# Kernel tuning notes

Measured on AMD Instinct MI355X. Metric: run time of the kernel, lower is better.

The kernel has to match this reference:

```python
import jax, jax.numpy as jnp
import numpy as np

NUM_PROPERTIES = 10000
HDIM = 512
OUTPUT_DIM = 2
BATCH = 512
NUM_PROPS = 128


def setup_inputs() -> dict:
    key = jax.random.key(0)
    k1, k2, k3, k4 = jax.random.split(key, 4)
    hidden_states = jax.random.normal(k1, (BATCH, NUM_PROPS, HDIM), dtype=jnp.float32)
    properties = jax.random.randint(k2, (BATCH, NUM_PROPS), 0, NUM_PROPERTIES, dtype=jnp.int64)
    mask = jnp.ones((BATCH, NUM_PROPS), dtype=jnp.float32)
    # learned params: per-property classifier weight (H, D) and bias (D)
    classifier_weights = jax.random.normal(k3, (NUM_PROPERTIES, HDIM, OUTPUT_DIM), dtype=jnp.float32) * 0.02
    classifier_bias = jax.random.normal(k4, (NUM_PROPERTIES, OUTPUT_DIM), dtype=jnp.float32) * 0.02
    return {
        "hidden_states": hidden_states,
        "properties": properties,
        "mask": mask,
        "classifier_weights": classifier_weights,
        "classifier_bias": classifier_bias,
    }


def reference(hidden_states, properties, mask, classifier_weights, classifier_bias):
    # gather per-(batch, prop) weight matrices and biases
    W = classifier_weights[properties]          # (B, P, H, D)
    b = classifier_bias[properties]             # (B, P, D)
    # (B,P,1,H) @ (B,P,H,D) -> (B,P,D)
    out = jnp.einsum("bph,bphd->bpd", hidden_states, W) + b
    out = out * mask[..., None]
    return out
```

## Files before the change

### kernel.cpp

```cpp
#include <hip/hip_runtime.h>


#define H 512
#define D 2
#define CAP 48
#define OVF_WAVES 256

__device__ __forceinline__ void gemv_one_bp(
    const float* __restrict__ hs, const float* __restrict__ mask,
    const float* __restrict__ W,  const float* __restrict__ bias,
    float* __restrict__ out, int bp, int prop, int lane)
{
    const float2* h2 = (const float2*)(hs + (size_t)bp * H);
    const float4* w4 = (const float4*)(W + (size_t)prop * (H * D));

    float2 ha = h2[lane];
    float2 hb = h2[64 + lane];
    float2 hc = h2[128 + lane];
    float2 hd = h2[192 + lane];
    float4 wa = w4[lane];
    float4 wb = w4[64 + lane];
    float4 wc = w4[128 + lane];
    float4 wd = w4[192 + lane];

    float s0 = ha.x * wa.x + ha.y * wa.z
             + hb.x * wb.x + hb.y * wb.z
             + hc.x * wc.x + hc.y * wc.z
             + hd.x * wd.x + hd.y * wd.z;
    float s1 = ha.x * wa.y + ha.y * wa.w
             + hb.x * wb.y + hb.y * wb.w
             + hc.x * wc.y + hc.y * wc.w
             + hd.x * wd.y + hd.y * wd.w;

    #pragma unroll
    for (int off = 32; off > 0; off >>= 1) {
        s0 += __shfl_xor(s0, off, 64);
        s1 += __shfl_xor(s1, off, 64);
    }

    if (lane == 0) {
        const float m  = mask[bp];
        const float b0 = bias[(size_t)prop * D + 0];
        const float b1 = bias[(size_t)prop * D + 1];
        float2 r;
        r.x = (s0 + b0) * m;
        r.y = (s1 + b1) * m;
        *(float2*)(out + (size_t)bp * D) = r;
    }
}

__global__ __launch_bounds__(256) void bucket_kernel(
    const int* __restrict__ props, int BP,
    int* __restrict__ counts,
    int* __restrict__ slots,
    int* __restrict__ ovf_cnt,
    int* __restrict__ ovf)
{
    int i = blockIdx.x * blockDim.x + threadIdx.x;
    const int stride = gridDim.x * blockDim.x;
    for (; i < BP; i += stride) {
        const int p = props[i];
        const int idx = atomicAdd(&counts[p], 1);
        if (idx < CAP) {
            slots[p * CAP + idx] = i;
        } else {
            const int o = atomicAdd(ovf_cnt, 1);
            ovf[o] = i;
        }
    }
}

__global__ __launch_bounds__(256) void per_prop_kernel(
    const float* __restrict__ hs,
    const int*   __restrict__ props,
    const float* __restrict__ mask,
    const float* __restrict__ W,
    const float* __restrict__ bias,
    float*       __restrict__ out,
    const int*   __restrict__ counts,
    const int*   __restrict__ slots,
    const int*   __restrict__ ovf_cnt,
    const int*   __restrict__ ovf,
    int nprop)
{
    const int wid  = (blockIdx.x * blockDim.x + threadIdx.x) >> 6;
    const int lane = threadIdx.x & 63;

    if (wid < nprop) {
        int cnt = counts[wid];
        if (cnt > CAP) cnt = CAP;
        if (cnt == 0) return;

        const float4* w4 = (const float4*)(W + (size_t)wid * (H * D));
        const float4 wa = w4[lane];
        const float4 wb = w4[64 + lane];
        const float4 wc = w4[128 + lane];
        const float4 wd = w4[192 + lane];
        const float b0 = bias[(size_t)wid * D + 0];
        const float b1 = bias[(size_t)wid * D + 1];

        const int myslot = (lane < cnt) ? slots[wid * CAP + lane] : 0;

        int bp = __shfl(myslot, 0, 64);
        const float2* h2 = (const float2*)(hs + (size_t)bp * H);
        float2 ha = h2[lane];
        float2 hb = h2[64 + lane];
        float2 hc = h2[128 + lane];
        float2 hd = h2[192 + lane];

        for (int j = 0; j < cnt; ++j) {
            const int bpn = __shfl(myslot, (j + 1 < 64) ? j + 1 : 0, 64);
            float2 na = make_float2(0.f, 0.f), nb = na, nc = na, nd = na;
            if (j + 1 < cnt) {
                const float2* hn = (const float2*)(hs + (size_t)bpn * H);
                na = hn[lane];
                nb = hn[64 + lane];
                nc = hn[128 + lane];
                nd = hn[192 + lane];
            }

            float s0 = ha.x * wa.x + ha.y * wa.z
                     + hb.x * wb.x + hb.y * wb.z
                     + hc.x * wc.x + hc.y * wc.z
                     + hd.x * wd.x + hd.y * wd.z;
            float s1 = ha.x * wa.y + ha.y * wa.w
                     + hb.x * wb.y + hb.y * wb.w
                     + hc.x * wc.y + hc.y * wc.w
                     + hd.x * wd.y + hd.y * wd.w;

            #pragma unroll
            for (int off = 32; off > 0; off >>= 1) {
                s0 += __shfl_xor(s0, off, 64);
                s1 += __shfl_xor(s1, off, 64);
            }

            if (lane == 0) {
                const float m = mask[bp];
                float2 r;
                r.x = (s0 + b0) * m;
                r.y = (s1 + b1) * m;
                *(float2*)(out + (size_t)bp * D) = r;
            }

            bp = bpn;
            ha = na; hb = nb; hc = nc; hd = nd;
        }
    } else {
        const int n = *ovf_cnt;
        for (int i = wid - nprop; i < n; i += OVF_WAVES) {
            const int bp = ovf[i];
            gemv_one_bp(hs, mask, W, bias, out, bp, props[bp], lane);
        }
    }
}

__global__ __launch_bounds__(256) void adapter_gemv_kernel(
    const float* __restrict__ hs,
    const int*   __restrict__ props,
    const float* __restrict__ mask,
    const float* __restrict__ W,
    const float* __restrict__ bias,
    float* __restrict__ out,
    int BP)
{
    const int tid  = blockIdx.x * blockDim.x + threadIdx.x;
    const int bp   = tid >> 6;
    const int lane = tid & 63;
    if (bp >= BP) return;
    gemv_one_bp(hs, mask, W, bias, out, bp, props[bp], lane);
}

extern "C" void kernel_launch(void* const* d_in, const int* in_sizes, int n_in,
                              void* d_out, int out_size, void* d_ws, size_t ws_size,
                              hipStream_t stream) {
    const float* hs    = (const float*)d_in[0];
    const int*   props = (const int*)d_in[1];
    const float* mask  = (const float*)d_in[2];
    const float* W     = (const float*)d_in[3];
    const float* bias  = (const float*)d_in[4];
    float* out = (float*)d_out;

    const int BP    = in_sizes[1];
    const int nprop = in_sizes[3] / (H * D);

    const size_t off_counts = 0;
    const size_t off_slots  = (((size_t)nprop * 4 + 4) + 255) & ~(size_t)255;
    const size_t off_ovf    = off_slots + (size_t)nprop * CAP * 4;
    const size_t ws_needed  = off_ovf + (size_t)BP * 4;

    if (ws_size < ws_needed) {
        const int threads = 256;
        const int blocks  = (BP * 64 + threads - 1) / threads;
        adapter_gemv_kernel<<<blocks, threads, 0, stream>>>(hs, props, mask, W, bias, out, BP);
        return;
    }

    int* counts  = (int*)((char*)d_ws + off_counts);
    int* ovf_cnt = counts + nprop;
    int* slots   = (int*)((char*)d_ws + off_slots);
    int* ovf     = (int*)((char*)d_ws + off_ovf);

    hipMemsetAsync(counts, 0, off_slots, stream);

    {
        const int threads = 256;
        int blocks = (BP + threads - 1) / threads;
        if (blocks > 1024) blocks = 1024;
        bucket_kernel<<<blocks, threads, 0, stream>>>(props, BP, counts, slots, ovf_cnt, ovf);
    }

    {
        const int threads     = 256;
        const int total_waves = nprop + OVF_WAVES;
        const int blocks      = (total_waves * 64 + threads - 1) / threads;
        per_prop_kernel<<<blocks, threads, 0, stream>>>(
            hs, props, mask, W, bias, out, counts, slots, ovf_cnt, ovf, nprop);
    }
}
```

Before: 49.06 us.

## Split each property's bucket across four waves of one block

Each property now gets a full 256-thread block instead of a single wave. The four waves take interleaved slots of that property's bucket, which cuts the serial chain per wave from about 6.5 rows to about 2. The overflow path is remapped to dedicated blocks. In exchange, each of the four waves loads the same weight slice again, though those loads should mostly hit in cache, and four times as many waves are launched, many of them exiting early when the bucket holds few rows.

```diff
diff --git a/kernel.cpp b/kernel.cpp
--- a/kernel.cpp
+++ b/kernel.cpp
@@ -4,7 +4,8 @@
 #define H 512
 #define D 2
 #define CAP 48
-#define OVF_WAVES 256
+#define KSPLIT 4
+#define OVF_BLOCKS 64
 
 __device__ __forceinline__ void gemv_one_bp(
     const float* __restrict__ hs, const float* __restrict__ mask,
@@ -83,23 +84,25 @@
     const int*   __restrict__ ovf,
     int nprop)
 {
-    const int wid  = (blockIdx.x * blockDim.x + threadIdx.x) >> 6;
+    const int k    = threadIdx.x >> 6;
     const int lane = threadIdx.x & 63;
 
-    if (wid < nprop) {
-        int cnt = counts[wid];
+    if (blockIdx.x < nprop) {
+        const int p = blockIdx.x;
+        int cnt = counts[p];
         if (cnt > CAP) cnt = CAP;
-        if (cnt == 0) return;
-
-        const float4* w4 = (const float4*)(W + (size_t)wid * (H * D));
+        if (k >= cnt) return;
+        const int nt = (cnt - k + KSPLIT - 1) / KSPLIT;
+
+        const float4* w4 = (const float4*)(W + (size_t)p * (H * D));
         const float4 wa = w4[lane];
         const float4 wb = w4[64 + lane];
         const float4 wc = w4[128 + lane];
         const float4 wd = w4[192 + lane];
-        const float b0 = bias[(size_t)wid * D + 0];
-        const float b1 = bias[(size_t)wid * D + 1];
-
-        const int myslot = (lane < cnt) ? slots[wid * CAP + lane] : 0;
+        const float b0 = bias[(size_t)p * D + 0];
+        const float b1 = bias[(size_t)p * D + 1];
+
+        const int myslot = (lane < nt) ? slots[p * CAP + k + KSPLIT * lane] : 0;
 
         int bp = __shfl(myslot, 0, 64);
         const float2* h2 = (const float2*)(hs + (size_t)bp * H);
@@ -108,10 +111,10 @@
         float2 hc = h2[128 + lane];
         float2 hd = h2[192 + lane];
 
-        for (int j = 0; j < cnt; ++j) {
-            const int bpn = __shfl(myslot, (j + 1 < 64) ? j + 1 : 0, 64);
+        for (int t = 0; t < nt; ++t) {
+            const int bpn = __shfl(myslot, (t + 1 < 64) ? t + 1 : 0, 64);
             float2 na = make_float2(0.f, 0.f), nb = na, nc = na, nd = na;
-            if (j + 1 < cnt) {
+            if (t + 1 < nt) {
                 const float2* hn = (const float2*)(hs + (size_t)bpn * H);
                 na = hn[lane];
                 nb = hn[64 + lane];
@@ -146,8 +149,9 @@
             ha = na; hb = nb; hc = nc; hd = nd;
         }
     } else {
+        const int w = (blockIdx.x - nprop) * KSPLIT + k;
         const int n = *ovf_cnt;
-        for (int i = wid - nprop; i < n; i += OVF_WAVES) {
+        for (int i = w; i < n; i += OVF_BLOCKS * KSPLIT) {
             const int bp = ovf[i];
             gemv_one_bp(hs, mask, W, bias, out, bp, props[bp], lane);
         }
@@ -210,9 +214,8 @@
     }
 
     {
-        const int threads     = 256;
-        const int total_waves = nprop + OVF_WAVES;
-        const int blocks      = (total_waves * 64 + threads - 1) / threads;
+        const int threads = 256;
+        const int blocks  = nprop + OVF_BLOCKS;
         per_prop_kernel<<<blocks, threads, 0, stream>>>(
             hs, props, mask, W, bias, out, counts, slots, ovf_cnt, ovf, nprop);
     }
```

Measured after the change: 44.21 us. 9.9% less time.
